# Kernel tuning notes

Measured on AMD Instinct MI355X. Metric: run time of the kernel, lower is better.

Reference implementation:

```python
import jax, jax.numpy as jnp
import numpy as np

B_SZ, SEQ, D_IN, D_HID, D_OUT = 32, 1024, 128, 256, 128
N_FREQ = SEQ // 2 + 1


def setup_inputs() -> dict:
    key = jax.random.key(0)
    ks = jax.random.split(key, 10)
    s_w = 1.0 / np.sqrt(D_IN)
    return {
        "x": jax.random.normal(ks[0], (B_SZ, SEQ, D_IN), dtype=jnp.float32),
        "W_re": jax.random.uniform(ks[1], (N_FREQ, D_IN, D_HID), minval=-s_w, maxval=s_w, dtype=jnp.float32),
        "W_im": jax.random.uniform(ks[2], (N_FREQ, D_IN, D_HID), minval=-s_w, maxval=s_w, dtype=jnp.float32),
        "B_re": jax.random.uniform(ks[3], (N_FREQ, D_HID), minval=-s_w, maxval=s_w, dtype=jnp.float32),
        "B_im": jax.random.uniform(ks[4], (N_FREQ, D_HID), minval=-s_w, maxval=s_w, dtype=jnp.float32),
        "W_rc": jax.random.uniform(ks[5], (D_IN, D_HID), minval=-s_w, maxval=s_w, dtype=jnp.float32),
        "fc1_w": jax.random.uniform(ks[6], (D_HID, D_HID), minval=-1/np.sqrt(D_HID), maxval=1/np.sqrt(D_HID), dtype=jnp.float32),
        "fc1_b": jnp.zeros((D_HID,), dtype=jnp.float32),
        "fc2_w": jax.random.uniform(ks[7], (D_HID, D_OUT), minval=-1/np.sqrt(D_HID), maxval=1/np.sqrt(D_HID), dtype=jnp.float32),
        "fc2_b": jnp.zeros((D_OUT,), dtype=jnp.float32),
    }


def reference(x, W_re, W_im, B_re, B_im, W_rc, fc1_w, fc1_b, fc2_w, fc2_b):
    # residual channel projection: [b,t,d] @ [d,k] -> [b,t,k]
    x_rc = jnp.einsum("btd,dk->btk", x, W_rc)
    # FFT-domain per-frequency complex MLP
    x_fft = jnp.fft.rfft(x, axis=1)  # [b, n_freq, d] complex
    W = W_re + 1j * W_im             # [n_freq, d, k]
    Bc = B_re + 1j * B_im            # [n_freq, k]
    out = jnp.einsum("bti,tio->bto", x_fft, W) + Bc
    # split-ReLU on real/imag parts, recombine as complex
    out = jax.nn.relu(out.real) + 1j * jax.nn.relu(out.imag)
    out = jnp.fft.irfft(out, n=x.shape[1], axis=1)  # [b, t, k] real
    out = out + x_rc
    # 2-layer MLP head with LeakyReLU (slope 0.01)
    h = jax.nn.leaky_relu(out @ fc1_w + fc1_b, negative_slope=0.01)
    return h @ fc2_w + fc2_b
```

## Files before the change

### kernel.cpp

```cpp
#include <hip/hip_runtime.h>
#include <math.h>

#define NB 32
#define NT 1024
#define ND 128
#define NK 256
#define NO 128
#define NF 513

#define PAD(e) ((e) + ((e) >> 4))

typedef __attribute__((ext_vector_type(8))) short bf16x8;
typedef __attribute__((ext_vector_type(4))) float f32x4;

__device__ __forceinline__ unsigned short f2bf(float f) {
  union { float f; unsigned u; } v; v.f = f;
  return (unsigned short)((v.u + 0x7fffu + ((v.u >> 16) & 1u)) >> 16);
}
__device__ __forceinline__ float bf2f(unsigned u) {
  union { unsigned u; float f; } v; v.u = u << 16;
  return v.f;
}
__device__ __forceinline__ unsigned packbf(float re, float im) {
  return (unsigned)f2bf(re) | ((unsigned)f2bf(im) << 16);
}
__device__ __forceinline__ unsigned digrev4(unsigned j) {
  unsigned r = __brev(j) >> 22;
  return ((r & 0x2AAu) >> 1) | ((r & 0x155u) << 1);
}

template <bool INV>
__device__ void fft1024_r4(float* __restrict__ ar, float* __restrict__ ai,
                           const float* __restrict__ twc,
                           const float* __restrict__ tws, int l) {
  for (int j = l; j < 1024; j += 64) {
    int r = (int)digrev4((unsigned)j);
    if (j < r) {
      int pj = PAD(j), pr = PAD(r);
      float t0 = ar[pj], t1 = ai[pj];
      ar[pj] = ar[pr]; ai[pj] = ai[pr];
      ar[pr] = t0; ai[pr] = t1;
    }
  }
#pragma unroll
  for (int s = 0; s < 5; ++s) {
    const int sh = 2 * s;
    const int q = 1 << sh;
#pragma unroll
    for (int it = 0; it < 4; ++it) {
      int m = it * 64 + l;
      int r = m & (q - 1);
      int i0 = ((m >> sh) << (sh + 2)) + r;
      int p0 = PAD(i0), p1 = PAD(i0 + q), p2 = PAD(i0 + 2 * q), p3 = PAD(i0 + 3 * q);
      float x0r = ar[p0], x0i = ai[p0];
      float x1r = ar[p1], x1i = ai[p1];
      float x2r = ar[p2], x2i = ai[p2];
      float x3r = ar[p3], x3i = ai[p3];
      float t1r, t1i, t2r, t2i, t3r, t3i;
      if (s == 0) {
        t1r = x1r; t1i = x1i; t2r = x2r; t2i = x2i; t3r = x3r; t3i = x3i;
      } else {
        int e = r << (8 - sh);
        float c1 = twc[e], s1 = tws[e];
        float c2 = c1 * c1 - s1 * s1, s2 = 2.0f * c1 * s1;
        float c3 = c1 * c2 - s1 * s2, s3 = c1 * s2 + s1 * c2;
        t1r = x1r * c1 - x1i * s1; t1i = x1r * s1 + x1i * c1;
        t2r = x2r * c2 - x2i * s2; t2i = x2r * s2 + x2i * c2;
        t3r = x3r * c3 - x3i * s3; t3i = x3r * s3 + x3i * c3;
      }
      float u0r = x0r + t2r, u0i = x0i + t2i;
      float u1r = x0r - t2r, u1i = x0i - t2i;
      float u2r = t1r + t3r, u2i = t1i + t3i;
      float u3r = t1r - t3r, u3i = t1i - t3i;
      ar[p0] = u0r + u2r; ai[p0] = u0i + u2i;
      ar[p2] = u0r - u2r; ai[p2] = u0i - u2i;
      if (INV) {
        ar[p1] = u1r - u3i; ai[p1] = u1i + u3r;
        ar[p3] = u1r + u3i; ai[p3] = u1i - u3r;
      } else {
        ar[p1] = u1r + u3i; ai[p1] = u1i - u3r;
        ar[p3] = u1r - u3i; ai[p3] = u1i + u3r;
      }
    }
  }
}

__global__ __launch_bounds__(512, 4) void rfft_kernel(const float* __restrict__ x,
                                                      unsigned* __restrict__ Xc) {
  __shared__ float ar[8 * 1088], ai_[8 * 1088];
  __shared__ float twc[768], tws[768];
  const int tid = threadIdx.x;
  const int b = blockIdx.x >> 3;
  const int c0 = (blockIdx.x & 7) << 4;
  for (int k = tid; k < 768; k += 512) {
    float s, c;
    sincosf(6.283185307179586f * (float)k / 1024.0f, &s, &c);
    twc[k] = c; tws[k] = -s;
  }
  const float* xb = x + (size_t)b * NT * ND + c0;
  for (int idx = tid; idx < 8192; idx += 512) {
    int t = idx >> 3, g = idx & 7;
    float2 v = *(const float2*)(xb + (size_t)t * ND + 2 * g);
    int p = g * 1088 + PAD(t);
    ar[p] = v.x; ai_[p] = v.y;
  }
  __syncthreads();
  const int g = tid >> 6, l = tid & 63;
  fft1024_r4<false>(ar + g * 1088, ai_ + g * 1088, twc, tws, l);
  __syncthreads();
  unsigned* Xb = Xc + (size_t)b * NF * ND + c0;
  for (int idx = tid; idx < NF * 8; idx += 512) {
    int f = idx >> 3, gg = idx & 7;
    int mr = (1024 - f) & 1023;
    int pf = gg * 1088 + PAD(f), pm = gg * 1088 + PAD(mr);
    float x1 = ar[pf], y1 = ai_[pf];
    float xr = ar[pm], yr = ai_[pm];
    unsigned e0 = packbf(0.5f * (x1 + xr), 0.5f * (y1 - yr));
    unsigned e1 = packbf(0.5f * (y1 + yr), 0.5f * (xr - x1));
    *(uint2*)(Xb + (size_t)f * ND + 2 * gg) = make_uint2(e0, e1);
  }
}

__global__ __launch_bounds__(512, 6) void freq_mfma_kernel(
    const unsigned* __restrict__ Xc, const float* __restrict__ Wre,
    const float* __restrict__ Wim, const float* __restrict__ Bre,
    const float* __restrict__ Bim, unsigned* __restrict__ Fc) {
  __shared__ unsigned short Wr_l[64 * 128], Wi_l[64 * 128];
  __shared__ unsigned short Xr_l[NB * ND], Xi_l[NB * ND];
  const int tid = threadIdx.x;
  const int f = blockIdx.x >> 2;
  const int n0 = (blockIdx.x & 3) << 6;

  {
    const int g = tid >> 4;
    const int cq = tid & 15;
    const float* w0 = Wre + (size_t)f * ND * NK + n0 + cq * 4;
    const float* w1 = Wim + (size_t)f * ND * NK + n0 + cq * 4;
#pragma unroll
    for (int w = 0; w < 2; ++w) {
      const float* wb = w ? w1 : w0;
      unsigned short* wl = w ? Wi_l : Wr_l;
      float4 r0 = *(const float4*)(wb + (size_t)(4 * g + 0) * NK);
      float4 r1 = *(const float4*)(wb + (size_t)(4 * g + 1) * NK);
      float4 r2 = *(const float4*)(wb + (size_t)(4 * g + 2) * NK);
      float4 r3 = *(const float4*)(wb + (size_t)(4 * g + 3) * NK);
      const float* c0 = (const float*)&r0;
      const float* c1 = (const float*)&r1;
      const float* c2 = (const float*)&r2;
      const float* c3 = (const float*)&r3;
#pragma unroll
      for (int j = 0; j < 4; ++j) {
        int nl = cq * 4 + j;
        int sw = (nl >> 2) ^ ((nl & 3) << 2);
        int off = nl * 128 + (((g >> 1) ^ sw) << 3) + ((g & 1) << 2);
        ushort4 v;
        v.x = f2bf(c0[j]); v.y = f2bf(c1[j]);
        v.z = f2bf(c2[j]); v.w = f2bf(c3[j]);
        *(ushort4*)&wl[off] = v;
      }
    }
  }
#pragma unroll
  for (int it = 0; it < 4; ++it) {
    int idx = it * 512 + tid;
    int bb = idx >> 6, dp = idx & 63;
    int d = dp * 2;
    uint2 u = *(const uint2*)(Xc + ((size_t)bb * NF + f) * ND + d);
    unsigned re2 = (u.x & 0xffffu) | (u.y << 16);
    unsigned im2 = (u.x >> 16) | (u.y & 0xffff0000u);
    int off = bb * 128 + ((((d >> 3) ^ (bb & 15))) << 3) + (d & 7);
    *(unsigned*)&Xr_l[off] = re2;
    *(unsigned*)&Xi_l[off] = im2;
  }
  __syncthreads();

  const int wv = tid >> 6, l = tid & 63;
  const int lr = l & 15, lg = l >> 4;
  const int wvn = wv & 3, mh = wv >> 2;
  const int nl = wvn * 16 + lr;
  const int swn = (nl >> 2) ^ ((nl & 3) << 2);
  const int row = mh * 16 + lr;
  f32x4 aR, aI;
  {
    float br = Bre[(size_t)f * NK + n0 + nl];
    float bi = Bim[(size_t)f * NK + n0 + nl];
    aR = (f32x4){br, br, br, br};
    aI = (f32x4){bi, bi, bi, bi};
  }
#pragma unroll
  for (int ks = 0; ks < 4; ++ks) {
    int kb = ks * 4 + lg;
    bf16x8 xr = *(const bf16x8*)&Xr_l[row * 128 + ((kb ^ lr) << 3)];
    bf16x8 xi = *(const bf16x8*)&Xi_l[row * 128 + ((kb ^ lr) << 3)];
    bf16x8 bR = *(const bf16x8*)&Wr_l[nl * 128 + ((kb ^ swn) << 3)];
    bf16x8 bI = *(const bf16x8*)&Wi_l[nl * 128 + ((kb ^ swn) << 3)];
    union { bf16x8 v; unsigned u[4]; } xiu, xnu;
    xiu.v = xi;
    xnu.u[0] = xiu.u[0] ^ 0x80008000u;
    xnu.u[1] = xiu.u[1] ^ 0x80008000u;
    xnu.u[2] = xiu.u[2] ^ 0x80008000u;
    xnu.u[3] = xiu.u[3] ^ 0x80008000u;
    aR = __builtin_amdgcn_mfma_f32_16x16x32_bf16(xr, bR, aR, 0, 0, 0);
    aR = __builtin_amdgcn_mfma_f32_16x16x32_bf16(xnu.v, bI, aR, 0, 0, 0);
    aI = __builtin_amdgcn_mfma_f32_16x16x32_bf16(xr, bI, aI, 0, 0, 0);
    aI = __builtin_amdgcn_mfma_f32_16x16x32_bf16(xi, bR, aI, 0, 0, 0);
  }
#pragma unroll
  for (int r = 0; r < 4; ++r) {
    int brow = mh * 16 + lg * 4 + r;
    float vR = fmaxf(aR[r], 0.0f);
    float vI = fmaxf(aI[r], 0.0f);
    Fc[((size_t)brow * NF + f) * NK + n0 + nl] = packbf(vR, vI);
  }
}

__global__ __launch_bounds__(512, 4) void irfft_kernel(const unsigned* __restrict__ Fc,
                                                       unsigned short* __restrict__ yf) {
  __shared__ float ar[8 * 1088], ai_[8 * 1088];
  __shared__ float twc[768], tws[768];
  const int tid = threadIdx.x;
  const int b = blockIdx.x >> 4;
  const int k0 = (blockIdx.x & 15) << 4;
  for (int k = tid; k < 768; k += 512) {
    float s, c;
    sincosf(6.283185307179586f * (float)k / 1024.0f, &s, &c);
    twc[k] = c; tws[k] = s;
  }
  for (int idx = tid; idx < 8192; idx += 512) {
    int f = idx >> 3, g = idx & 7;
    int src = (f <= 512) ? f : 1024 - f;
    uint2 u = *(const uint2*)(Fc + ((size_t)b * NF + src) * NK + k0 + 2 * g);
    float arr = bf2f(u.x & 0xffff), ari = bf2f(u.x >> 16);
    float brr = bf2f(u.y & 0xffff), bri = bf2f(u.y >> 16);
    float zr, zi;
    if (f <= 512) { zr = arr - bri; zi = ari + brr; }
    else          { zr = arr + bri; zi = brr - ari; }
    int p = g * 1088 + PAD(f);
    ar[p] = zr; ai_[p] = zi;
  }
  __syncthreads();
  const int g = tid >> 6, l = tid & 63;
  fft1024_r4<true>(ar + g * 1088, ai_ + g * 1088, twc, tws, l);
  __syncthreads();
  const float sc = 1.0f / 1024.0f;
  unsigned* yb = (unsigned*)(yf + (size_t)b * NT * NK + k0);
  for (int idx = tid; idx < 8192; idx += 512) {
    int t = idx >> 3, gg = idx & 7;
    int p = gg * 1088 + PAD(t);
    yb[(size_t)t * (NK / 2) + gg] = packbf(ar[p] * sc, ai_[p] * sc);
  }
}

__global__ __launch_bounds__(256) void wconv_kernel(const float* __restrict__ Wrc,
                                                    const float* __restrict__ W1,
                                                    const float* __restrict__ W2,
                                                    unsigned short* __restrict__ Wt) {
  int i = blockIdx.x * 256 + threadIdx.x;
  if (i < 32768) {
    int k = i >> 8, n = i & 255;
    Wt[n * 128 + k] = f2bf(Wrc[i]);
  } else if (i < 98304) {
    int j = i - 32768; int k = j >> 8, n = j & 255;
    Wt[32768 + n * 256 + k] = f2bf(W1[j]);
  } else if (i < 131072) {
    int j = i - 98304; int k = j >> 7, n = j & 127;
    Wt[98304 + n * 256 + k] = f2bf(W2[j]);
  }
}

__global__ __launch_bounds__(512, 4) void mlp_fused_kernel(
    const float* __restrict__ x, const unsigned short* __restrict__ yf,
    const unsigned short* __restrict__ Wt, const float* __restrict__ b1,
    const float* __restrict__ b2, float* __restrict__ out) {
  __shared__ unsigned short y_l[64 * 256];
  __shared__ unsigned short u_l[64 * 256];
  const int tid = threadIdx.x;
  const int wv = tid >> 6, l = tid & 63;
  const int lr = l & 15, lg = l >> 4;
  const int row0 = blockIdx.x * 64;
  const unsigned short* W1_t = Wt + 32768;
  const unsigned short* W2_t = Wt + 98304;

#pragma unroll
  for (int it = 0; it < 4; ++it) {
    int idx = it * 512 + tid;
    int row = idx >> 5, c4 = idx & 31;
    float4 v = *(const float4*)(x + (size_t)(row0 + row) * ND + c4 * 4);
    int blk = (c4 >> 1) ^ (row & 15);
    unsigned short* p = &u_l[row * 128 + blk * 8 + (c4 & 1) * 4];
    p[0] = f2bf(v.x); p[1] = f2bf(v.y); p[2] = f2bf(v.z); p[3] = f2bf(v.w);
  }
  __syncthreads();

  f32x4 acc[4][2];
#pragma unroll
  for (int m = 0; m < 4; ++m)
#pragma unroll
    for (int nt = 0; nt < 2; ++nt) acc[m][nt] = (f32x4){0.f, 0.f, 0.f, 0.f};
#pragma unroll
  for (int ks = 0; ks < 4; ++ks) {
    bf16x8 bb[2];
#pragma unroll
    for (int nt = 0; nt < 2; ++nt) {
      int col = wv * 32 + nt * 16 + lr;
      bb[nt] = *(const bf16x8*)&Wt[col * 128 + ks * 32 + lg * 8];
    }
    bf16x8 aa[4];
#pragma unroll
    for (int m = 0; m < 4; ++m) {
      int row = m * 16 + lr;
      aa[m] = *(const bf16x8*)&u_l[row * 128 + (((ks * 4 + lg) ^ (row & 15)) << 3)];
    }
#pragma unroll
    for (int m = 0; m < 4; ++m)
#pragma unroll
      for (int nt = 0; nt < 2; ++nt)
        acc[m][nt] = __builtin_amdgcn_mfma_f32_16x16x32_bf16(aa[m], bb[nt], acc[m][nt], 0, 0, 0);
  }
#pragma unroll
  for (int m = 0; m < 4; ++m)
#pragma unroll
    for (int nt = 0; nt < 2; ++nt)
#pragma unroll
      for (int r = 0; r < 4; ++r) {
        int row = m * 16 + lg * 4 + r;
        int col = wv * 32 + nt * 16 + lr;
        float v = acc[m][nt][r] + bf2f(yf[(size_t)(row0 + row) * NK + col]);
        int blk = (col >> 3) ^ (row & 31);
        y_l[row * 256 + blk * 8 + (col & 7)] = f2bf(v);
      }
  __syncthreads();

  f32x4 a2[4][2];
  {
    float bv0 = b1[wv * 32 + lr], bv1 = b1[wv * 32 + 16 + lr];
#pragma unroll
    for (int m = 0; m < 4; ++m) {
      a2[m][0] = (f32x4){bv0, bv0, bv0, bv0};
      a2[m][1] = (f32x4){bv1, bv1, bv1, bv1};
    }
  }
#pragma unroll
  for (int ks = 0; ks < 8; ++ks) {
    bf16x8 bb[2];
#pragma unroll
    for (int nt = 0; nt < 2; ++nt) {
      int col = wv * 32 + nt * 16 + lr;
      bb[nt] = *(const bf16x8*)&W1_t[col * 256 + ks * 32 + lg * 8];
    }
    bf16x8 aa[4];
#pragma unroll
    for (int m = 0; m < 4; ++m) {
      int row = m * 16 + lr;
      aa[m] = *(const bf16x8*)&y_l[row * 256 + (((ks * 4 + lg) ^ (row & 31)) << 3)];
    }
#pragma unroll
    for (int m = 0; m < 4; ++m)
#pragma unroll
      for (int nt = 0; nt < 2; ++nt)
        a2[m][nt] = __builtin_amdgcn_mfma_f32_16x16x32_bf16(aa[m], bb[nt], a2[m][nt], 0, 0, 0);
  }
#pragma unroll
  for (int m = 0; m < 4; ++m)
#pragma unroll
    for (int nt = 0; nt < 2; ++nt)
#pragma unroll
      for (int r = 0; r < 4; ++r) {
        int row = m * 16 + lg * 4 + r;
        int col = wv * 32 + nt * 16 + lr;
        float v = a2[m][nt][r];
        v = (v > 0.0f) ? v : 0.01f * v;
        int blk = (col >> 3) ^ (row & 31);
        u_l[row * 256 + blk * 8 + (col & 7)] = f2bf(v);
      }
  __syncthreads();

  const int col3 = wv * 16 + lr;
  f32x4 a3[4];
  {
    float bv = b2[col3];
#pragma unroll
    for (int m = 0; m < 4; ++m) a3[m] = (f32x4){bv, bv, bv, bv};
  }
#pragma unroll
  for (int ks = 0; ks < 8; ++ks) {
    bf16x8 bb = *(const bf16x8*)&W2_t[col3 * 256 + ks * 32 + lg * 8];
    bf16x8 aa[4];
#pragma unroll
    for (int m = 0; m < 4; ++m) {
      int row = m * 16 + lr;
      aa[m] = *(const bf16x8*)&u_l[row * 256 + (((ks * 4 + lg) ^ (row & 31)) << 3)];
    }
#pragma unroll
    for (int m = 0; m < 4; ++m)
      a3[m] = __builtin_amdgcn_mfma_f32_16x16x32_bf16(aa[m], bb, a3[m], 0, 0, 0);
  }
#pragma unroll
  for (int m = 0; m < 4; ++m)
#pragma unroll
    for (int r = 0; r < 4; ++r) {
      int row = m * 16 + lg * 4 + r;
      out[(size_t)(row0 + row) * NO + col3] = a3[m][r];
    }
}

extern "C" void kernel_launch(void* const* d_in, const int* in_sizes, int n_in,
                              void* d_out, int out_size, void* d_ws, size_t ws_size,
                              hipStream_t stream) {
  const float* x     = (const float*)d_in[0];
  const float* W_re  = (const float*)d_in[1];
  const float* W_im  = (const float*)d_in[2];
  const float* B_re  = (const float*)d_in[3];
  const float* B_im  = (const float*)d_in[4];
  const float* W_rc  = (const float*)d_in[5];
  const float* fc1_w = (const float*)d_in[6];
  const float* fc1_b = (const float*)d_in[7];
  const float* fc2_w = (const float*)d_in[8];
  const float* fc2_b = (const float*)d_in[9];
  float* out = (float*)d_out;

  const size_t SZ_X = (size_t)NB * NF * ND;
  const size_t SZ_F = (size_t)NB * NF * NK;
  const size_t SZ_Y = (size_t)NB * NT * NK;
  unsigned* Xc = (unsigned*)d_ws;
  unsigned* Fc = Xc + SZ_X;
  unsigned short* yf = (unsigned short*)(Fc + SZ_F);
  unsigned short* Wt = yf + SZ_Y;

  wconv_kernel<<<dim3(512), dim3(256), 0, stream>>>(W_rc, fc1_w, fc2_w, Wt);
  rfft_kernel<<<dim3(NB * 8), dim3(512), 0, stream>>>(x, Xc);
  freq_mfma_kernel<<<dim3(NF * 4), dim3(512), 0, stream>>>(Xc, W_re, W_im, B_re, B_im, Fc);
  irfft_kernel<<<dim3(NB * 16), dim3(512), 0, stream>>>(Fc, yf);
  mlp_fused_kernel<<<dim3((NB * NT) / 64), dim3(512), 0, stream>>>(x, yf, Wt, fc1_b, fc2_b, out);
}
```

Baseline: 103.7 us.

## Make freq GEMM kernel persistent over frequencies with double-buffered weight prefetch

Each block now handles 9 consecutive frequencies for one 64-column slice instead of one frequency. The next frequency's fp32 weights are prefetched into registers while the current one computes, and they are staged into a double-buffered LDS tile. X operands are read straight from global memory into registers rather than through LDS. The aim is to hide weight-load latency and cut per-block launch and sync overhead, but the grid drops to 228 blocks, which may underfill the GPU's compute units and limit memory parallelism.

```diff
diff --git a/kernel.cpp b/kernel.cpp
--- a/kernel.cpp
+++ b/kernel.cpp
@@ -121,96 +121,112 @@
   }
 }
 
-__global__ __launch_bounds__(512, 6) void freq_mfma_kernel(
+#define FPB 9
+__global__ __launch_bounds__(512, 2) void freq_mfma_kernel(
     const unsigned* __restrict__ Xc, const float* __restrict__ Wre,
     const float* __restrict__ Wim, const float* __restrict__ Bre,
     const float* __restrict__ Bim, unsigned* __restrict__ Fc) {
-  __shared__ unsigned short Wr_l[64 * 128], Wi_l[64 * 128];
-  __shared__ unsigned short Xr_l[NB * ND], Xi_l[NB * ND];
+  __shared__ unsigned short Wl[2][2][64 * 128];
   const int tid = threadIdx.x;
-  const int f = blockIdx.x >> 2;
-  const int n0 = (blockIdx.x & 3) << 6;
-
-  {
-    const int g = tid >> 4;
-    const int cq = tid & 15;
-    const float* w0 = Wre + (size_t)f * ND * NK + n0 + cq * 4;
-    const float* w1 = Wim + (size_t)f * ND * NK + n0 + cq * 4;
-#pragma unroll
-    for (int w = 0; w < 2; ++w) {
-      const float* wb = w ? w1 : w0;
-      unsigned short* wl = w ? Wi_l : Wr_l;
-      float4 r0 = *(const float4*)(wb + (size_t)(4 * g + 0) * NK);
-      float4 r1 = *(const float4*)(wb + (size_t)(4 * g + 1) * NK);
-      float4 r2 = *(const float4*)(wb + (size_t)(4 * g + 2) * NK);
-      float4 r3 = *(const float4*)(wb + (size_t)(4 * g + 3) * NK);
-      const float* c0 = (const float*)&r0;
-      const float* c1 = (const float*)&r1;
-      const float* c2 = (const float*)&r2;
-      const float* c3 = (const float*)&r3;
-#pragma unroll
-      for (int j = 0; j < 4; ++j) {
-        int nl = cq * 4 + j;
-        int sw = (nl >> 2) ^ ((nl & 3) << 2);
-        int off = nl * 128 + (((g >> 1) ^ sw) << 3) + ((g & 1) << 2);
-        ushort4 v;
-        v.x = f2bf(c0[j]); v.y = f2bf(c1[j]);
-        v.z = f2bf(c2[j]); v.w = f2bf(c3[j]);
-        *(ushort4*)&wl[off] = v;
-      }
-    }
-  }
-#pragma unroll
-  for (int it = 0; it < 4; ++it) {
-    int idx = it * 512 + tid;
-    int bb = idx >> 6, dp = idx & 63;
-    int d = dp * 2;
-    uint2 u = *(const uint2*)(Xc + ((size_t)bb * NF + f) * ND + d);
-    unsigned re2 = (u.x & 0xffffu) | (u.y << 16);
-    unsigned im2 = (u.x >> 16) | (u.y & 0xffff0000u);
-    int off = bb * 128 + ((((d >> 3) ^ (bb & 15))) << 3) + (d & 7);
-    *(unsigned*)&Xr_l[off] = re2;
-    *(unsigned*)&Xi_l[off] = im2;
-  }
-  __syncthreads();
-
+  const int qg = blockIdx.x & 3;
+  const int fg = blockIdx.x >> 2;
+  const int n0 = qg << 6;
+  const int f0 = fg * FPB;
+  const int count = (f0 + FPB <= NF) ? FPB : (NF - f0);
+
+  const int sg = tid >> 4;
+  const int scq = tid & 15;
   const int wv = tid >> 6, l = tid & 63;
   const int lr = l & 15, lg = l >> 4;
   const int wvn = wv & 3, mh = wv >> 2;
   const int nl = wvn * 16 + lr;
   const int swn = (nl >> 2) ^ ((nl & 3) << 2);
   const int row = mh * 16 + lr;
-  f32x4 aR, aI;
-  {
+
+  float4 wreg[8];
+
+  auto issueW = [&](int f) {
+    const float* wr = Wre + (size_t)f * ND * NK + n0 + scq * 4;
+    const float* wi = Wim + (size_t)f * ND * NK + n0 + scq * 4;
+#pragma unroll
+    for (int r = 0; r < 4; ++r) wreg[r] = *(const float4*)(wr + (size_t)(4 * sg + r) * NK);
+#pragma unroll
+    for (int r = 0; r < 4; ++r) wreg[4 + r] = *(const float4*)(wi + (size_t)(4 * sg + r) * NK);
+  };
+  auto stageW = [&](int buf) {
+#pragma unroll
+    for (int w = 0; w < 2; ++w) {
+      unsigned short* wl = Wl[buf][w];
+      const float* c0 = (const float*)&wreg[w * 4 + 0];
+      const float* c1 = (const float*)&wreg[w * 4 + 1];
+      const float* c2 = (const float*)&wreg[w * 4 + 2];
+      const float* c3 = (const float*)&wreg[w * 4 + 3];
+#pragma unroll
+      for (int j = 0; j < 4; ++j) {
+        int nn = scq * 4 + j;
+        int sw = (nn >> 2) ^ ((nn & 3) << 2);
+        int off = nn * 128 + (((sg >> 1) ^ sw) << 3) + ((sg & 1) << 2);
+        ushort4 v;
+        v.x = f2bf(c0[j]); v.y = f2bf(c1[j]);
+        v.z = f2bf(c2[j]); v.w = f2bf(c3[j]);
+        *(ushort4*)&wl[off] = v;
+      }
+    }
+  };
+
+  issueW(f0);
+  for (int i = 0; i < count; ++i) {
+    const int f = f0 + i;
+    const int buf = i & 1;
+    stageW(buf);
+    __syncthreads();
+
+    uint4 xreg[8];
+    {
+      const unsigned* xb = Xc + ((size_t)row * NF + f) * ND + lg * 8;
+#pragma unroll
+      for (int ks = 0; ks < 4; ++ks) {
+        xreg[2 * ks] = *(const uint4*)(xb + ks * 32);
+        xreg[2 * ks + 1] = *(const uint4*)(xb + ks * 32 + 4);
+      }
+    }
     float br = Bre[(size_t)f * NK + n0 + nl];
     float bi = Bim[(size_t)f * NK + n0 + nl];
-    aR = (f32x4){br, br, br, br};
-    aI = (f32x4){bi, bi, bi, bi};
-  }
-#pragma unroll
-  for (int ks = 0; ks < 4; ++ks) {
-    int kb = ks * 4 + lg;
-    bf16x8 xr = *(const bf16x8*)&Xr_l[row * 128 + ((kb ^ lr) << 3)];
-    bf16x8 xi = *(const bf16x8*)&Xi_l[row * 128 + ((kb ^ lr) << 3)];
-    bf16x8 bR = *(const bf16x8*)&Wr_l[nl * 128 + ((kb ^ swn) << 3)];
-    bf16x8 bI = *(const bf16x8*)&Wi_l[nl * 128 + ((kb ^ swn) << 3)];
-    union { bf16x8 v; unsigned u[4]; } xiu, xnu;
-    xiu.v = xi;
-    xnu.u[0] = xiu.u[0] ^ 0x80008000u;
-    xnu.u[1] = xiu.u[1] ^ 0x80008000u;
-    xnu.u[2] = xiu.u[2] ^ 0x80008000u;
-    xnu.u[3] = xiu.u[3] ^ 0x80008000u;
-    aR = __builtin_amdgcn_mfma_f32_16x16x32_bf16(xr, bR, aR, 0, 0, 0);
-    aR = __builtin_amdgcn_mfma_f32_16x16x32_bf16(xnu.v, bI, aR, 0, 0, 0);
-    aI = __builtin_amdgcn_mfma_f32_16x16x32_bf16(xr, bI, aI, 0, 0, 0);
-    aI = __builtin_amdgcn_mfma_f32_16x16x32_bf16(xi, bR, aI, 0, 0, 0);
-  }
-#pragma unroll
-  for (int r = 0; r < 4; ++r) {
-    int brow = mh * 16 + lg * 4 + r;
-    float vR = fmaxf(aR[r], 0.0f);
-    float vI = fmaxf(aI[r], 0.0f);
-    Fc[((size_t)brow * NF + f) * NK + n0 + nl] = packbf(vR, vI);
+    if (i + 1 < count) issueW(f + 1);
+
+    f32x4 aR = (f32x4){br, br, br, br};
+    f32x4 aI = (f32x4){bi, bi, bi, bi};
+#pragma unroll
+    for (int ks = 0; ks < 4; ++ks) {
+      int kb = ks * 4 + lg;
+      uint4 a0 = xreg[2 * ks], a1 = xreg[2 * ks + 1];
+      union { bf16x8 v; unsigned u[4]; } xr, xi, xn;
+      xr.u[0] = (a0.x & 0xffffu) | (a0.y << 16);
+      xr.u[1] = (a0.z & 0xffffu) | (a0.w << 16);
+      xr.u[2] = (a1.x & 0xffffu) | (a1.y << 16);
+      xr.u[3] = (a1.z & 0xffffu) | (a1.w << 16);
+      xi.u[0] = (a0.x >> 16) | (a0.y & 0xffff0000u);
+      xi.u[1] = (a0.z >> 16) | (a0.w & 0xffff0000u);
+      xi.u[2] = (a1.x >> 16) | (a1.y & 0xffff0000u);
+      xi.u[3] = (a1.z >> 16) | (a1.w & 0xffff0000u);
+      xn.u[0] = xi.u[0] ^ 0x80008000u;
+      xn.u[1] = xi.u[1] ^ 0x80008000u;
+      xn.u[2] = xi.u[2] ^ 0x80008000u;
+      xn.u[3] = xi.u[3] ^ 0x80008000u;
+      bf16x8 bR = *(const bf16x8*)&Wl[buf][0][nl * 128 + ((kb ^ swn) << 3)];
+      bf16x8 bI = *(const bf16x8*)&Wl[buf][1][nl * 128 + ((kb ^ swn) << 3)];
+      aR = __builtin_amdgcn_mfma_f32_16x16x32_bf16(xr.v, bR, aR, 0, 0, 0);
+      aR = __builtin_amdgcn_mfma_f32_16x16x32_bf16(xn.v, bI, aR, 0, 0, 0);
+      aI = __builtin_amdgcn_mfma_f32_16x16x32_bf16(xr.v, bI, aI, 0, 0, 0);
+      aI = __builtin_amdgcn_mfma_f32_16x16x32_bf16(xi.v, bR, aI, 0, 0, 0);
+    }
+#pragma unroll
+    for (int r = 0; r < 4; ++r) {
+      int brow = mh * 16 + lg * 4 + r;
+      float vR = fmaxf(aR[r], 0.0f);
+      float vI = fmaxf(aI[r], 0.0f);
+      Fc[((size_t)brow * NF + f) * NK + n0 + nl] = packbf(vR, vI);
+    }
   }
 }
 
@@ -429,7 +445,7 @@
 
   wconv_kernel<<<dim3(512), dim3(256), 0, stream>>>(W_rc, fc1_w, fc2_w, Wt);
   rfft_kernel<<<dim3(NB * 8), dim3(512), 0, stream>>>(x, Xc);
-  freq_mfma_kernel<<<dim3(NF * 4), dim3(512), 0, stream>>>(Xc, W_re, W_im, B_re, B_im, Fc);
+  freq_mfma_kernel<<<dim3(4 * 57), dim3(512), 0, stream>>>(Xc, W_re, W_im, B_re, B_im, Fc);
   irfft_kernel<<<dim3(NB * 16), dim3(512), 0, stream>>>(Fc, yf);
   mlp_fused_kernel<<<dim3((NB * NT) / 64), dim3(512), 0, stream>>>(x, yf, Wt, fc1_b, fc2_b, out);
 }
```

Measured after the change: 119.5 us. +15.3%, slower.
